# Performance work log

Measured on AMD Instinct MI355X. Metric: run time of the kernel, lower is better.

## Reference

```python
import jax, jax.numpy as jnp
import numpy as np

N_NODES = 100000
N_EDGES = 1600000
F_IN = 64
F_OUT = 64
N_BASES = 8
GRID_LO, GRID_HI = -1.0, 1.0
LN_EPS = 1e-5


def setup_inputs() -> dict:
    key = jax.random.key(0)
    k1, k2, k3, k4 = jax.random.split(key, 4)
    x = jax.random.normal(k1, (N_NODES, F_IN), dtype=jnp.float32)
    edge_index = jax.random.randint(k2, (2, N_EDGES), 0, N_NODES, dtype=jnp.int64)
    edge_weight = jax.random.uniform(k3, (N_EDGES,), dtype=jnp.float32)
    scale = 1.0 / np.sqrt(F_IN * N_BASES)
    weights = jax.random.uniform(k4, (F_IN, N_BASES, F_OUT), dtype=jnp.float32,
                                 minval=-scale, maxval=scale)
    return {
        "x": x,
        "edge_index": edge_index,
        "edge_weight": edge_weight,
        "ln_gamma": jnp.ones((F_IN,), jnp.float32),
        "ln_beta": jnp.zeros((F_IN,), jnp.float32),
        "weights": weights,
        "bias": jnp.zeros((F_OUT,), jnp.float32),
    }


def reference(x, edge_index, edge_weight, ln_gamma, ln_beta, weights, bias):
    n = x.shape[0]
    src, dst = edge_index[0], edge_index[1]
    # add self loops
    loop = jnp.arange(n, dtype=src.dtype)
    src_a = jnp.concatenate([src, loop])
    dst_a = jnp.concatenate([dst, loop])
    w = jnp.concatenate([edge_weight, jnp.ones((n,), x.dtype)])
    # row (out-degree over src) normalization
    deg = jax.ops.segment_sum(w, src_a, num_segments=n)
    deg = jnp.maximum(deg, 1.0)
    w = w / deg[src_a]
    # agg[i] = sum_{edges src=i} w * x[dst]  (sparse COO matmul)
    agg = jax.ops.segment_sum(w[:, None] * x[dst_a], src_a, num_segments=n)
    # FastKAN: LayerNorm -> RBF expansion -> einsum contraction
    mu = jnp.mean(agg, axis=-1, keepdims=True)
    var = jnp.mean((agg - mu) ** 2, axis=-1, keepdims=True)
    h = (agg - mu) * jax.lax.rsqrt(var + LN_EPS) * ln_gamma + ln_beta
    centers = jnp.linspace(GRID_LO, GRID_HI, N_BASES, dtype=x.dtype)
    sigma = (GRID_HI - GRID_LO) / (N_BASES - 1) / 2.0
    denom = 2.0 * sigma * sigma
    phi = jnp.exp(-((h[..., None] - centers) ** 2) / denom)  # (N, F_IN, N_BASES)
    out = jnp.einsum('nib,ibo->no', phi, weights) + bias
    return out
```

## Files before the change

### kernel.cpp

```cpp
#include <hip/hip_runtime.h>
#include <hip/hip_bf16.h>
#include <cstdint>

#define N_NODES 100000
#define N_EDGESC 1600000
#define FDIM 64
#define KDIM 512
#define CAP 48
#define BINSHIFT 5
#define BINSZ 32
#define NBINS 3125
#define BINCAP 768
#define EPB 4096

typedef __attribute__((ext_vector_type(8))) short short8;
typedef __attribute__((ext_vector_type(4))) float float4v;
typedef __attribute__((ext_vector_type(4))) unsigned uint4v;

__device__ __forceinline__ float bf2f(unsigned short u) {
    return __uint_as_float(((unsigned)u) << 16);
}
__device__ __forceinline__ unsigned short f2bf(float f) {
    unsigned u = __float_as_uint(f);
    u += 0x7FFFu + ((u >> 16) & 1u);
    return (unsigned short)(u >> 16);
}
template <int ISBF>
__device__ __forceinline__ float ldx(const void* p, long i) {
    return ISBF ? bf2f(((const unsigned short*)p)[i]) : ((const float*)p)[i];
}
template <int IS64>
__device__ __forceinline__ int ldi(const void* p, long i) {
    return IS64 ? (int)((const long long*)p)[i] : ((const int*)p)[i];
}

__global__ void k_detect(const unsigned* __restrict__ x, const unsigned* __restrict__ ei,
                         int* __restrict__ flags, unsigned* __restrict__ g_binofs) {
    int t = threadIdx.x;
    for (int b = t; b < NBINS; b += 256) g_binofs[b] = 0;
    if (t < 64) {
        unsigned xv = x[t];
        int lowexp = (int)((xv >> 7) & 0xFFu);
        int okbf = (lowexp >= 100 && lowexp <= 140) ? 1 : 0;
        unsigned ov = ei[2 * t + 1];
        int zero = (ov == 0u) ? 1 : 0;
#pragma unroll
        for (int off = 1; off < 64; off <<= 1) {
            okbf += __shfl_xor(okbf, off);
            zero += __shfl_xor(zero, off);
        }
        if (t == 0) {
            flags[0] = (okbf >= 48) ? 1 : 0;
            flags[1] = (zero >= 48) ? 1 : 0;
        }
    }
}

__global__ __launch_bounds__(256) void k_stage(const void* __restrict__ x,
                                               const int* __restrict__ flags,
                                               unsigned short* __restrict__ xs) {
    long g = (long)blockIdx.x * 256 + threadIdx.x;
    if (g >= (long)N_NODES * 16) return;
    if (flags[0]) {
        ((ushort4*)xs)[g] = ((const ushort4*)x)[g];
    } else {
        float4 v = ((const float4*)x)[g];
        ushort4 o;
        o.x = f2bf(v.x); o.y = f2bf(v.y); o.z = f2bf(v.z); o.w = f2bf(v.w);
        ((ushort4*)xs)[g] = o;
    }
}

template <int ISBF, int IS64>
__device__ __forceinline__ void part_impl(const void* ei, const void* ew,
                                          unsigned* g_binofs, uint2* part,
                                          unsigned* hist, unsigned* base,
                                          int tid, int blk) {
    for (int b = tid; b < NBINS; b += 256) hist[b] = 0;
    __syncthreads();

    unsigned binv[16];
    uint2 rec[16];
    int valid[16];
#pragma unroll
    for (int it = 0; it < 16; ++it) {
        long e = (long)blk * EPB + it * 256 + tid;
        valid[it] = e < N_EDGESC;
        binv[it] = 0; rec[it] = make_uint2(0u, 0u);
        if (valid[it]) {
            unsigned src = (unsigned)ldi<IS64>(ei, e);
            unsigned dst = (unsigned)ldi<IS64>(ei, (long)N_EDGESC + e);
            float w = ldx<ISBF>(ew, e);
            w = fminf(fmaxf(w, 0.0f), 0.99996f);
            unsigned q = (unsigned)(w * 32768.0f + 0.5f);
            if (q > 32767u) q = 32767u;
            binv[it] = src >> BINSHIFT;
            rec[it] = make_uint2(dst | (q << 17), src & (BINSZ - 1));
            atomicAdd(&hist[binv[it]], 1u);
        }
    }
    __syncthreads();
    for (int b = tid; b < NBINS; b += 256) {
        unsigned cc = hist[b];
        base[b] = cc ? atomicAdd(&g_binofs[b], cc) : 0u;
        hist[b] = 0;
    }
    __syncthreads();
#pragma unroll
    for (int it = 0; it < 16; ++it) {
        if (valid[it]) {
            unsigned rk = atomicAdd(&hist[binv[it]], 1u);
            unsigned pos = base[binv[it]] + rk;
            if (pos < BINCAP) part[(size_t)binv[it] * BINCAP + pos] = rec[it];
        }
    }
}

__global__ __launch_bounds__(256) void k_part_all(const void* __restrict__ ei,
                                                  const void* __restrict__ ew,
                                                  const int* __restrict__ flags,
                                                  unsigned* __restrict__ g_binofs,
                                                  uint2* __restrict__ part) {
    __shared__ unsigned hist[NBINS];
    __shared__ unsigned base[NBINS];
    int isbf = flags[0], is64 = flags[1];
    int tid = threadIdx.x, blk = blockIdx.x;
    if (is64) {
        if (isbf) part_impl<1, 1>(ei, ew, g_binofs, part, hist, base, tid, blk);
        else      part_impl<0, 1>(ei, ew, g_binofs, part, hist, base, tid, blk);
    } else {
        if (isbf) part_impl<1, 0>(ei, ew, g_binofs, part, hist, base, tid, blk);
        else      part_impl<0, 0>(ei, ew, g_binofs, part, hist, base, tid, blk);
    }
}

__global__ void k_pack(const void* __restrict__ w, const int* __restrict__ flags,
                       unsigned short* __restrict__ bp) {
    int g = blockIdx.x * blockDim.x + threadIdx.x;
    int isbf = flags[0];
    unsigned short v = isbf ? ((const unsigned short*)w)[g] : f2bf(((const float*)w)[g]);
    int k = g >> 6, o = g & 63;
    int kstep = k >> 5, quad = (k >> 3) & 3, j = k & 7;
    bp[((kstep * 64 + o) * 4 + quad) * 8 + j] = v;
}

__global__ __launch_bounds__(256) void k_bin_all(
    const unsigned short* __restrict__ xs, const unsigned* __restrict__ g_binofs,
    const uint2* __restrict__ part, float* __restrict__ agg) {
    __shared__ unsigned lists[BINSZ * CAP];
    __shared__ unsigned lcnt[BINSZ];
    int tid = threadIdx.x, bin = blockIdx.x;
    if (tid < BINSZ) lcnt[tid] = 0;
    __syncthreads();

    unsigned cntb = g_binofs[bin];
    if (cntb > BINCAP) cntb = BINCAP;
    const uint2* recs = part + (size_t)bin * BINCAP;
    for (unsigned j = tid; j < cntb; j += 256) {
        uint2 r = recs[j];
        int sl = (int)(r.y & (BINSZ - 1));
        unsigned idx = atomicAdd(&lcnt[sl], 1u);
        if (idx < CAP) lists[sl * CAP + idx] = r.x;
    }
    __syncthreads();

    int wave = tid >> 6, lane = tid & 63;
    int qw = wave * 4 + (lane >> 4);
    int q = lane & 15;
    for (int n = qw; n < BINSZ; n += 16) {
        int node = (bin << BINSHIFT) + n;
        if (node >= N_NODES) continue;
        ushort4 xr0 = ((const ushort4*)xs)[(size_t)node * 16 + q];
        float a0 = bf2f(xr0.x), a1 = bf2f(xr0.y), a2 = bf2f(xr0.z), a3 = bf2f(xr0.w);
        float sumw = 0.f;
        unsigned m = lcnt[n];
        if (m > CAP) m = CAP;
        const unsigned* lst = lists + n * CAP;
        for (unsigned j = 0; j < m; j += 16) {
            unsigned ee[16];
            float xlo[16], xmi[16], xma[16], xhi[16];
#pragma unroll
            for (int i = 0; i < 16; ++i) {
                unsigned jj = j + (unsigned)i;
                ee[i] = lst[jj < m ? jj : m - 1];
            }
#pragma unroll
            for (int i = 0; i < 16; ++i) {
                unsigned dst = ee[i] & 0x1FFFFu;
                ushort4 xr = ((const ushort4*)xs)[(size_t)dst * 16 + q];
                xlo[i] = bf2f(xr.x); xmi[i] = bf2f(xr.y);
                xma[i] = bf2f(xr.z); xhi[i] = bf2f(xr.w);
            }
#pragma unroll
            for (int i = 0; i < 16; ++i) {
                float w = (j + (unsigned)i < m) ? (float)(ee[i] >> 17) * (1.0f / 32768.0f) : 0.f;
                sumw += w;
                a0 += w * xlo[i]; a1 += w * xmi[i];
                a2 += w * xma[i]; a3 += w * xhi[i];
            }
        }
        float inv = 1.0f / (1.0f + sumw);
        ((float4*)agg)[(size_t)node * 16 + q] = make_float4(a0 * inv, a1 * inv, a2 * inv, a3 * inv);
    }
}

#define RBF_S 5.945252531f
#define HS_LD 68

template <int ISBF>
__device__ __forceinline__ void fused_impl(
    const float* agg, const void* gamma, const void* beta,
    const unsigned short* bp, const void* bias, void* out,
    float (&hs)[64 * HS_LD], int tid, int blk) {
    int r = tid >> 2;
    int c0 = (tid & 3) << 4;
    int gr = blk * 64 + r;
    float vals[16];
    float s1 = 0.f, s2 = 0.f;
    if (gr < N_NODES) {
        const float4* p = (const float4*)(agg + (long)gr * FDIM + c0);
#pragma unroll
        for (int q = 0; q < 4; ++q) {
            float4 t = p[q];
            vals[q * 4 + 0] = t.x; vals[q * 4 + 1] = t.y;
            vals[q * 4 + 2] = t.z; vals[q * 4 + 3] = t.w;
        }
#pragma unroll
        for (int j = 0; j < 16; ++j) { s1 += vals[j]; s2 += vals[j] * vals[j]; }
    }
    s1 += __shfl_xor(s1, 1); s1 += __shfl_xor(s1, 2);
    s2 += __shfl_xor(s2, 1); s2 += __shfl_xor(s2, 2);
    float mean = s1 * (1.0f / 64.0f);
    float var = s2 * (1.0f / 64.0f) - mean * mean;
    float rstd = rsqrtf(var + 1e-5f);
#pragma unroll
    for (int j = 0; j < 16; ++j) {
        int c = c0 + j;
        float hv = 0.f;
        if (gr < N_NODES)
            hv = (vals[j] - mean) * rstd * ldx<ISBF>(gamma, c) + ldx<ISBF>(beta, c);
        hs[r * HS_LD + c] = hv;
    }
    __syncthreads();

    int wv = tid >> 6, lane = tid & 63;
    int m = lane & 15, quad = lane >> 4;
    const float* hrow = hs + (wv * 16 + m) * HS_LD;

    float hvv[16];
#pragma unroll
    for (int ks = 0; ks < 16; ++ks) hvv[ks] = hrow[ks * 4 + quad];

    float4v z = {0.f, 0.f, 0.f, 0.f};
    float4v acc[4];
#pragma unroll
    for (int ct = 0; ct < 4; ++ct) acc[ct] = z;

#pragma unroll
    for (int ks = 0; ks < 16; ++ks) {
        float hv = hvv[ks];
        unsigned e[8];
#pragma unroll
        for (int j = 0; j < 8; ++j) {
            float dj = -(-1.0f + (float)j * (2.0f / 7.0f)) * RBF_S;
            float s = __builtin_fmaf(hv, RBF_S, dj);
            float p = exp2f(-(s * s));
            e[j] = __float_as_uint(p) + 0x8000u;
        }
        uint4v pk;
        pk.x = __builtin_amdgcn_perm(e[1], e[0], 0x07060302u);
        pk.y = __builtin_amdgcn_perm(e[3], e[2], 0x07060302u);
        pk.z = __builtin_amdgcn_perm(e[5], e[4], 0x07060302u);
        pk.w = __builtin_amdgcn_perm(e[7], e[6], 0x07060302u);
        short8 a = __builtin_bit_cast(short8, pk);
#pragma unroll
        for (int ct = 0; ct < 4; ++ct) {
            const short8* bptr =
                (const short8*)(bp + ((size_t)(ks * 64 + ct * 16 + m) * 4 + quad) * 8);
            short8 b = *bptr;
            acc[ct] = __builtin_amdgcn_mfma_f32_16x16x32_bf16(a, b, acc[ct], 0, 0, 0);
        }
    }

    int base_node = blk * 64 + wv * 16 + quad * 4;
#pragma unroll
    for (int ct = 0; ct < 4; ++ct) {
        float bb = ldx<ISBF>(bias, ct * 16 + m);
#pragma unroll
        for (int reg = 0; reg < 4; ++reg) {
            int node = base_node + reg;
            if (node < N_NODES) {
                float v = acc[ct][reg] + bb;
                long oi = (long)node * FDIM + ct * 16 + m;
                if (ISBF) ((unsigned short*)out)[oi] = f2bf(v);
                else      ((float*)out)[oi] = v;
            }
        }
    }
}

__global__ __launch_bounds__(256, 6) void k_fused(
    const float* __restrict__ agg, const void* __restrict__ gamma,
    const void* __restrict__ beta, const unsigned short* __restrict__ bp,
    const void* __restrict__ bias, const int* __restrict__ flags,
    void* __restrict__ out) {
    __shared__ float hs[64 * HS_LD];
    if (flags[0]) fused_impl<1>(agg, gamma, beta, bp, bias, out, hs, threadIdx.x, blockIdx.x);
    else          fused_impl<0>(agg, gamma, beta, bp, bias, out, hs, threadIdx.x, blockIdx.x);
}

extern "C" void kernel_launch(void* const* d_in, const int* in_sizes, int n_in,
                              void* d_out, int out_size, void* d_ws, size_t ws_size,
                              hipStream_t stream) {
    const void* x    = d_in[0];
    const void* ei   = d_in[1];
    const void* ew   = d_in[2];
    const void* gam  = d_in[3];
    const void* bet  = d_in[4];
    const void* wts  = d_in[5];
    const void* bias = d_in[6];

    char* ws = (char*)d_ws;
    unsigned* g_binofs = (unsigned*)ws;
    uint2*    part     = (uint2*)(ws + 16384);
    float*    agg      = (float*)(ws + 16384 + (size_t)NBINS * BINCAP * 8);
    unsigned short* bpw = (unsigned short*)((char*)agg + (size_t)N_NODES * FDIM * 4);
    int*      flags    = (int*)((char*)bpw + (size_t)KDIM * FDIM * 2);
    unsigned short* xstage = (unsigned short*)((char*)flags + 256);

    k_detect<<<1, 256, 0, stream>>>((const unsigned*)x, (const unsigned*)ei, flags, g_binofs);
    k_stage<<<(N_NODES * 16 + 255) / 256, 256, 0, stream>>>(x, flags, xstage);
    int pgrid = (N_EDGESC + EPB - 1) / EPB;
    k_part_all<<<pgrid, 256, 0, stream>>>(ei, ew, flags, g_binofs, part);
    k_pack<<<(KDIM * FDIM) / 256, 256, 0, stream>>>(wts, flags, bpw);
    k_bin_all<<<NBINS, 256, 0, stream>>>(xstage, g_binofs, part, agg);
    k_fused<<<(N_NODES + 63) / 64, 256, 0, stream>>>(agg, gam, bet, bpw, bias, flags, d_out);
}
```

Measured before the change: 209.4 us.

## Replace shared-histogram edge partition with direct global-atomic scatter; use native exp2

The edge partitioning kernel no longer builds a per-block shared-memory histogram with block-level offset reservation. Instead, a grid-stride loop does one global atomicAdd per edge on the bin counter and writes the record directly. This removes the large LDS footprint, the three barriers and the two-pass structure, at the cost of about 1.6M contended global atomics on 3125 counters. Separately, the RBF exponent uses the hardware exp2 builtin instead of exp2f, dropping range handling.

```diff
diff --git a/kernel.cpp b/kernel.cpp
--- a/kernel.cpp
+++ b/kernel.cpp
@@ -11,7 +11,7 @@
 #define BINSZ 32
 #define NBINS 3125
 #define BINCAP 768
-#define EPB 4096
+#define SCATBLK 2048
 
 typedef __attribute__((ext_vector_type(8))) short short8;
 typedef __attribute__((ext_vector_type(4))) float float4v;
@@ -72,65 +72,37 @@
 }
 
 template <int ISBF, int IS64>
-__device__ __forceinline__ void part_impl(const void* ei, const void* ew,
+__device__ __forceinline__ void scat_impl(const void* ei, const void* ew,
                                           unsigned* g_binofs, uint2* part,
-                                          unsigned* hist, unsigned* base,
-                                          int tid, int blk) {
-    for (int b = tid; b < NBINS; b += 256) hist[b] = 0;
-    __syncthreads();
-
-    unsigned binv[16];
-    uint2 rec[16];
-    int valid[16];
-#pragma unroll
-    for (int it = 0; it < 16; ++it) {
-        long e = (long)blk * EPB + it * 256 + tid;
-        valid[it] = e < N_EDGESC;
-        binv[it] = 0; rec[it] = make_uint2(0u, 0u);
-        if (valid[it]) {
-            unsigned src = (unsigned)ldi<IS64>(ei, e);
-            unsigned dst = (unsigned)ldi<IS64>(ei, (long)N_EDGESC + e);
-            float w = ldx<ISBF>(ew, e);
-            w = fminf(fmaxf(w, 0.0f), 0.99996f);
-            unsigned q = (unsigned)(w * 32768.0f + 0.5f);
-            if (q > 32767u) q = 32767u;
-            binv[it] = src >> BINSHIFT;
-            rec[it] = make_uint2(dst | (q << 17), src & (BINSZ - 1));
-            atomicAdd(&hist[binv[it]], 1u);
-        }
-    }
-    __syncthreads();
-    for (int b = tid; b < NBINS; b += 256) {
-        unsigned cc = hist[b];
-        base[b] = cc ? atomicAdd(&g_binofs[b], cc) : 0u;
-        hist[b] = 0;
-    }
-    __syncthreads();
-#pragma unroll
-    for (int it = 0; it < 16; ++it) {
-        if (valid[it]) {
-            unsigned rk = atomicAdd(&hist[binv[it]], 1u);
-            unsigned pos = base[binv[it]] + rk;
-            if (pos < BINCAP) part[(size_t)binv[it] * BINCAP + pos] = rec[it];
-        }
-    }
-}
-
-__global__ __launch_bounds__(256) void k_part_all(const void* __restrict__ ei,
-                                                  const void* __restrict__ ew,
-                                                  const int* __restrict__ flags,
-                                                  unsigned* __restrict__ g_binofs,
-                                                  uint2* __restrict__ part) {
-    __shared__ unsigned hist[NBINS];
-    __shared__ unsigned base[NBINS];
+                                          long g, long stride) {
+    for (long e = g; e < N_EDGESC; e += stride) {
+        unsigned src = (unsigned)ldi<IS64>(ei, e);
+        unsigned dst = (unsigned)ldi<IS64>(ei, (long)N_EDGESC + e);
+        float w = ldx<ISBF>(ew, e);
+        w = fminf(fmaxf(w, 0.0f), 0.99996f);
+        unsigned q = (unsigned)(w * 32768.0f + 0.5f);
+        if (q > 32767u) q = 32767u;
+        unsigned bin = src >> BINSHIFT;
+        unsigned pos = atomicAdd(&g_binofs[bin], 1u);
+        if (pos < BINCAP)
+            part[(size_t)bin * BINCAP + pos] = make_uint2(dst | (q << 17), src & (BINSZ - 1));
+    }
+}
+
+__global__ __launch_bounds__(256) void k_scat(const void* __restrict__ ei,
+                                              const void* __restrict__ ew,
+                                              const int* __restrict__ flags,
+                                              unsigned* __restrict__ g_binofs,
+                                              uint2* __restrict__ part) {
     int isbf = flags[0], is64 = flags[1];
-    int tid = threadIdx.x, blk = blockIdx.x;
+    long g = (long)blockIdx.x * 256 + threadIdx.x;
+    long stride = (long)SCATBLK * 256;
     if (is64) {
-        if (isbf) part_impl<1, 1>(ei, ew, g_binofs, part, hist, base, tid, blk);
-        else      part_impl<0, 1>(ei, ew, g_binofs, part, hist, base, tid, blk);
+        if (isbf) scat_impl<1, 1>(ei, ew, g_binofs, part, g, stride);
+        else      scat_impl<0, 1>(ei, ew, g_binofs, part, g, stride);
     } else {
-        if (isbf) part_impl<1, 0>(ei, ew, g_binofs, part, hist, base, tid, blk);
-        else      part_impl<0, 0>(ei, ew, g_binofs, part, hist, base, tid, blk);
+        if (isbf) scat_impl<1, 0>(ei, ew, g_binofs, part, g, stride);
+        else      scat_impl<0, 0>(ei, ew, g_binofs, part, g, stride);
     }
 }
 
@@ -264,7 +236,7 @@
         for (int j = 0; j < 8; ++j) {
             float dj = -(-1.0f + (float)j * (2.0f / 7.0f)) * RBF_S;
             float s = __builtin_fmaf(hv, RBF_S, dj);
-            float p = exp2f(-(s * s));
+            float p = __builtin_amdgcn_exp2f(-(s * s));
             e[j] = __float_as_uint(p) + 0x8000u;
         }
         uint4v pk;
@@ -330,8 +302,7 @@
 
     k_detect<<<1, 256, 0, stream>>>((const unsigned*)x, (const unsigned*)ei, flags, g_binofs);
     k_stage<<<(N_NODES * 16 + 255) / 256, 256, 0, stream>>>(x, flags, xstage);
-    int pgrid = (N_EDGESC + EPB - 1) / EPB;
-    k_part_all<<<pgrid, 256, 0, stream>>>(ei, ew, flags, g_binofs, part);
+    k_scat<<<SCATBLK, 256, 0, stream>>>(ei, ew, flags, g_binofs, part);
     k_pack<<<(KDIM * FDIM) / 256, 256, 0, stream>>>(wts, flags, bpw);
     k_bin_all<<<NBINS, 256, 0, stream>>>(xstage, g_binofs, part, agg);
     k_fused<<<(N_NODES + 63) / 64, 256, 0, stream>>>(agg, gam, bet, bpw, bias, flags, d_out);
```

Measured after the change: 314.2 us. 1.5x slower.
